# Kernel tuning notes

Hardware: AMD Instinct MI355X
Metric: run time of the kernel (lower is better)

## Reference

```python
import jax, jax.numpy as jnp
import numpy as np
import math

B, T, D, H, DM = 2, 2048, 1024, 16, 256
DK = D // H

def setup_inputs() -> dict:
    key = jax.random.key(0)
    ks = jax.random.split(key, 13)
    s = 0.02
    return {
        "Hx": jax.random.normal(ks[0], (B, D, T, 1), jnp.float32),
        "Hf": jax.random.normal(ks[1], (B, T, D), jnp.float32),
        "Gm": jax.random.normal(ks[2], (B, T, DM), jnp.float32),
        "Wg": jax.random.normal(ks[3], (T, DM), jnp.float32) * s,
        "bg": jax.random.normal(ks[4], (T,), jnp.float32) * s,
        "Wq": jax.random.normal(ks[5], (D, 2 * D), jnp.float32) * s,
        "bq": jax.random.normal(ks[6], (D,), jnp.float32) * s,
        "Wk": jax.random.normal(ks[7], (D, 2 * D), jnp.float32) * s,
        "bk": jax.random.normal(ks[8], (D,), jnp.float32) * s,
        "Wv": jax.random.normal(ks[9], (D, D), jnp.float32) * s,
        "bv": jax.random.normal(ks[10], (D,), jnp.float32) * s,
        "Wo": jax.random.normal(ks[11], (D, D), jnp.float32) * s,
        "bo": jax.random.normal(ks[12], (D,), jnp.float32) * s,
    }

def reference(Hx, Hf, Gm, Wg, bg, Wq, bq, Wk, bk, Wv, bv, Wo, bo):
    # Hx: (B, D, T, 1) -> (B, T, D)
    hx = jnp.transpose(Hx[..., 0], (0, 2, 1))
    h_cat = jnp.concatenate([hx, Hf], axis=-1)          # (B, T, 2D)
    Q = h_cat @ Wq.T + bq                               # (B, T, D)
    K = h_cat @ Wk.T + bk
    V = hx @ Wv.T + bv
    # split heads: (B, H, T, DK)
    Q = Q.reshape(B, T, H, DK).transpose(0, 2, 1, 3)
    K = K.reshape(B, T, H, DK).transpose(0, 2, 1, 3)
    V = V.reshape(B, T, H, DK).transpose(0, 2, 1, 3)
    scores = jnp.einsum('bhqd,bhkd->bhqk', Q, K) / math.sqrt(DK)
    bias = Gm @ Wg.T + bg                                # (B, T, T)
    scores = scores + bias[:, None, :, :]
    attn = jax.nn.softmax(scores, axis=-1)
    out = jnp.einsum('bhqk,bhkd->bhqd', attn, V)
    out = out.transpose(0, 2, 1, 3).reshape(B, T, D)
    return out @ Wo.T + bo
```

## Files before the change

### kernel.cpp

```cpp
#include <hip/hip_runtime.h>
#include <hip/hip_bf16.h>

using bf16 = __hip_bfloat16;
typedef __attribute__((ext_vector_type(8))) __bf16 bf16x8;
typedef __attribute__((ext_vector_type(4))) float f32x4;

#define GLB_AS(p) ((const __attribute__((address_space(1))) unsigned int*)(p))
#define LDS_AS(p) ((__attribute__((address_space(3))) unsigned int*)(p))

__device__ __forceinline__ void async_copy16(const void* g, void* l) {
  __builtin_amdgcn_global_load_lds(GLB_AS(g), LDS_AS(l), 16, 0, 0);
}

__device__ __forceinline__ f32x4 mfma16x16x32(bf16x8 a, bf16x8 b, f32x4 c) {
  return __builtin_amdgcn_mfma_f32_16x16x32_bf16(a, b, c, 0, 0, 0);
}

__device__ __forceinline__ float bfu2f(unsigned short u) {
  union { unsigned int i; float f; } x;
  x.i = (unsigned int)u << 16;
  return x.f;
}

#define LOG2E 1.44269504f

__global__ __launch_bounds__(256) void pack_hx(const float* __restrict__ Hx,
                                               bf16* __restrict__ hcat) {
  __shared__ float tile[64][65];
  const int t0 = blockIdx.x * 64, d0 = blockIdx.y * 64, b = blockIdx.z;
  const int c = threadIdx.x & 63, r0 = threadIdx.x >> 6;
#pragma unroll
  for (int i = 0; i < 16; ++i) {
    const int rd = r0 + i * 4;
    tile[rd][c] = Hx[((size_t)(b * 1024 + d0 + rd)) * 2048 + t0 + c];
  }
  __syncthreads();
#pragma unroll
  for (int i = 0; i < 16; ++i) {
    const int ct = r0 + i * 4;
    hcat[((size_t)(b * 2048 + t0 + ct)) * 2048 + d0 + c] =
        __float2bfloat16(tile[c][ct]);
  }
}

__global__ __launch_bounds__(256) void pack_all(
    const float* __restrict__ Hf, const float* __restrict__ Wq,
    const float* __restrict__ Wk, const float* __restrict__ Wv,
    const float* __restrict__ Wo, const float* __restrict__ Wg,
    const float* __restrict__ Gm, const float* __restrict__ bq,
    const float* __restrict__ bk, const float* __restrict__ bv,
    bf16* __restrict__ hcat, bf16* __restrict__ Wqkvb, bf16* __restrict__ Wob,
    bf16* __restrict__ Wgb, bf16* __restrict__ Gmb,
    float* __restrict__ qkvbias) {
  const int gid = blockIdx.x * 256 + threadIdx.x;
  const float* src = nullptr;
  bf16* dst = nullptr;
  int lg = 0, ldo = 0, off = 0, idx = 0;
  bool zero = false;
  if (gid < 1048576) { idx = gid; src = Hf; dst = hcat; lg = 8; ldo = 2048; off = 1024; }
  else if (gid < 1572864) { idx = gid - 1048576; src = Wq; dst = Wqkvb; lg = 9; ldo = 2048; }
  else if (gid < 2097152) { idx = gid - 1572864; src = Wk; dst = Wqkvb + (size_t)1024 * 2048; lg = 9; ldo = 2048; }
  else if (gid < 2359296) { idx = gid - 2097152; src = Wv; dst = Wqkvb + (size_t)2048 * 2048; lg = 8; ldo = 2048; }
  else if (gid < 2621440) { idx = gid - 2359296; zero = true; dst = Wqkvb + (size_t)2048 * 2048 + 1024; lg = 8; ldo = 2048; }
  else if (gid < 2883584) { idx = gid - 2621440; src = Wo; dst = Wob; lg = 8; ldo = 1024; }
  else if (gid < 3014656) { idx = gid - 2883584; src = Wg; dst = Wgb; lg = 6; ldo = 256; }
  else if (gid < 3276800) { idx = gid - 3014656; src = Gm; dst = Gmb; lg = 6; ldo = 256; }
  else if (gid < 3277056) { const int i = gid - 3276800; ((float4*)qkvbias)[i] = ((const float4*)bq)[i]; return; }
  else if (gid < 3277312) { const int i = gid - 3277056; ((float4*)(qkvbias + 1024))[i] = ((const float4*)bk)[i]; return; }
  else { const int i = gid - 3277312; ((float4*)(qkvbias + 2048))[i] = ((const float4*)bv)[i]; return; }
  const int row = idx >> lg, c = idx & ((1 << lg) - 1);
  bf16* o = dst + (size_t)row * ldo + off + c * 4;
  __align__(8) bf16 tmp[4];
  if (zero) {
    tmp[0] = tmp[1] = tmp[2] = tmp[3] = __float2bfloat16(0.f);
  } else {
    const float4 v = ((const float4*)src)[(size_t)idx];
    tmp[0] = __float2bfloat16(v.x); tmp[1] = __float2bfloat16(v.y);
    tmp[2] = __float2bfloat16(v.z); tmp[3] = __float2bfloat16(v.w);
  }
  *(ushort4*)o = *(const ushort4*)tmp;
}

__global__ __launch_bounds__(512, 2) void gemm_qkv_bias(
    const bf16* __restrict__ hcat, const bf16* __restrict__ Wqkv,
    const float* __restrict__ qkvbias, const bf16* __restrict__ Gmb,
    const bf16* __restrict__ Wgb, const float* __restrict__ bg,
    bf16* __restrict__ QKb, bf16* __restrict__ Vt, bf16* __restrict__ biasS) {
  __shared__ __align__(16) bf16 AS[2][256][64];
  __shared__ __align__(16) bf16 BS[2][256][64];
  const int lin = blockIdx.x;
  const bool isqkv = lin < 192;
  int m0, n0, Kd, KT, nit2;
  const bf16 *Ag, *Bg;
  const float* biasv;
  if (isqkv) {
    const int xcd = lin & 7, kk = lin >> 3;
    const int mloc = kk / 6, nloc = kk - mloc * 6;
    m0 = ((xcd >> 1) * 4 + mloc) * 256;
    n0 = ((xcd & 1) * 6 + nloc) * 256;
    Ag = hcat; Bg = Wqkv; biasv = qkvbias;
    Kd = 2048; KT = 32; nit2 = 16;
  } else {
    const int l2 = lin - 192;
    m0 = (l2 >> 3) * 256;
    n0 = (l2 & 7) * 256;
    Ag = Gmb; Bg = Wgb; biasv = bg;
    Kd = 256; KT = 4; nit2 = 2;
  }
  const int tid = threadIdx.x, lane = tid & 63, w = tid >> 6;
  const int w8 = w * 8, ln3 = lane >> 3, ch = lane & 7;
  const int fr = lane & 15, ck = lane >> 4;
  const int wm64 = (w >> 2) * 64;
  const int wn32 = (w & 3) * 32;

  f32x4 acc[8][4];
  const f32x4 fzero = {0.f, 0.f, 0.f, 0.f};
#pragma unroll
  for (int i = 0; i < 8; ++i)
#pragma unroll
    for (int j = 0; j < 4; ++j) acc[i][j] = fzero;

  auto stageA = [&](int buf, int mh, int kt) {
    const int k0 = kt * 64;
#pragma unroll
    for (int l = 0; l < 2; ++l) {
      const int rit = mh * 128 + l * 64 + w8 + ln3;
      async_copy16(Ag + (size_t)(m0 + rit) * Kd + k0 + ((ch ^ ln3) << 3),
                   (char*)&AS[buf][0][0] + ((mh * 128 + l * 64 + w8) << 7));
    }
  };
  auto stageB = [&](int buf, int nh, int kt) {
    const int k0 = kt * 64;
#pragma unroll
    for (int l = 0; l < 2; ++l) {
      const int rit = nh * 128 + l * 64 + w8 + ln3;
      async_copy16(Bg + (size_t)(n0 + rit) * Kd + k0 + ((ch ^ ln3) << 3),
                   (char*)&BS[buf][0][0] + ((nh * 128 + l * 64 + w8) << 7));
    }
  };

  bf16x8 af[4][2], bA[2][2], bB[2][2];
  auto ldA = [&](int buf, int mh) {
#pragma unroll
    for (int i = 0; i < 4; ++i)
#pragma unroll
      for (int ks = 0; ks < 2; ++ks)
        af[i][ks] = *(const bf16x8*)(
            &AS[buf][mh * 128 + wm64 + i * 16 + fr][0] +
            (((ks * 4 + ck) ^ (fr & 7)) << 3));
  };
  auto ldB = [&](bf16x8 (&dst)[2][2], int buf, int nh) {
#pragma unroll
    for (int j = 0; j < 2; ++j)
#pragma unroll
      for (int ks = 0; ks < 2; ++ks)
        dst[j][ks] = *(const bf16x8*)(
            &BS[buf][nh * 128 + wn32 + j * 16 + fr][0] +
            (((ks * 4 + ck) ^ (fr & 7)) << 3));
  };

#define BAR() __builtin_amdgcn_s_barrier()
#define LGKM0() asm volatile("s_waitcnt lgkmcnt(0)" ::: "memory")
#define MMAQ(MH, NH, BF)                                                      \
  __builtin_amdgcn_s_setprio(1);                                              \
  _Pragma("unroll") for (int i_ = 0; i_ < 4; ++i_) {                          \
    _Pragma("unroll") for (int j_ = 0; j_ < 2; ++j_) {                        \
      acc[(MH) * 4 + i_][(NH) * 2 + j_] = mfma16x16x32(                       \
          af[i_][0], BF[j_][0], acc[(MH) * 4 + i_][(NH) * 2 + j_]);           \
      acc[(MH) * 4 + i_][(NH) * 2 + j_] = mfma16x16x32(                       \
          af[i_][1], BF[j_][1], acc[(MH) * 4 + i_][(NH) * 2 + j_]);           \
    }                                                                         \
  }                                                                           \
  __builtin_amdgcn_s_setprio(0);

  stageA(0, 0, 0); stageB(0, 0, 0); stageB(0, 1, 0); stageA(0, 1, 0);
  stageA(1, 0, 1); stageB(1, 0, 1);
  asm volatile("s_waitcnt vmcnt(4)" ::: "memory");
  BAR();

  for (int it = 0; it < nit2; ++it) {
    const int kodd = 2 * it + 1;
    const int kn0 = (2 * it + 2 < KT) ? 2 * it + 2 : KT - 1;
    const int kn1 = (2 * it + 3 < KT) ? 2 * it + 3 : KT - 1;

    ldA(0, 0); ldB(bA, 0, 0);
    stageB(1, 1, kodd);
    asm volatile("s_waitcnt lgkmcnt(8)");
    BAR(); LGKM0();
    MMAQ(0, 0, bA);
    BAR();
    ldB(bB, 0, 1);
    stageA(1, 1, kodd);
    BAR(); LGKM0();
    MMAQ(0, 1, bB);
    BAR();
    ldA(0, 1);
    stageA(0, 0, kn0);
    BAR(); LGKM0();
    MMAQ(1, 0, bA);
    BAR();
    stageB(0, 0, kn0);
    asm volatile("s_waitcnt vmcnt(4)" ::: "memory");
    BAR();
    MMAQ(1, 1, bB);
    BAR();
    ldA(1, 0); ldB(bA, 1, 0);
    stageB(0, 1, kn0);
    asm volatile("s_waitcnt lgkmcnt(8)");
    BAR(); LGKM0();
    MMAQ(0, 0, bA);
    BAR();
    ldB(bB, 1, 1);
    stageA(0, 1, kn0);
    BAR(); LGKM0();
    MMAQ(0, 1, bB);
    BAR();
    ldA(1, 1);
    stageA(1, 0, kn1);
    BAR(); LGKM0();
    MMAQ(1, 0, bA);
    BAR();
    stageB(1, 0, kn1);
    asm volatile("s_waitcnt vmcnt(4)" ::: "memory");
    BAR();
    MMAQ(1, 1, bB);
    BAR();
  }
  asm volatile("s_waitcnt vmcnt(0)" ::: "memory");

  const int erow = (lane >> 4) * 4, ecol = lane & 15;
  if (!isqkv) {
#pragma unroll
    for (int ai = 0; ai < 8; ++ai) {
      const int gm0 = m0 + (ai >> 2) * 128 + wm64 + (ai & 3) * 16 + erow;
#pragma unroll
      for (int bj = 0; bj < 4; ++bj) {
        const int gn = n0 + (bj >> 1) * 128 + wn32 + (bj & 1) * 16 + ecol;
        const float bv = biasv[gn];
#pragma unroll
        for (int r = 0; r < 4; ++r)
          biasS[(size_t)(gm0 + r) * 2048 + gn] =
              __float2bfloat16((acc[ai][bj][r] + bv) * LOG2E);
      }
    }
  } else if (n0 < 2048) {
    const float sc = (n0 < 1024) ? 0.125f * LOG2E : 1.0f;
#pragma unroll
    for (int ai = 0; ai < 8; ++ai) {
      const int gm0 = m0 + (ai >> 2) * 128 + wm64 + (ai & 3) * 16 + erow;
#pragma unroll
      for (int bj = 0; bj < 4; ++bj) {
        const int gn = n0 + (bj >> 1) * 128 + wn32 + (bj & 1) * 16 + ecol;
        const float bv = biasv[gn];
#pragma unroll
        for (int r = 0; r < 4; ++r)
          QKb[(size_t)(gm0 + r) * 2048 + gn] =
              __float2bfloat16((acc[ai][bj][r] + bv) * sc);
      }
    }
  } else {
#pragma unroll
    for (int ai = 0; ai < 8; ++ai) {
      const int gm0 = m0 + (ai >> 2) * 128 + wm64 + (ai & 3) * 16 + erow;
      const int bb = gm0 >> 11;
      const int t = gm0 & 2047;
#pragma unroll
      for (int bj = 0; bj < 4; ++bj) {
        const int gn = n0 + (bj >> 1) * 128 + wn32 + (bj & 1) * 16 + ecol;
        const float bv = biasv[gn];
        const int d = gn - 2048;
        __align__(8) bf16 tmp[4];
#pragma unroll
        for (int r = 0; r < 4; ++r)
          tmp[r] = __float2bfloat16(acc[ai][bj][r] + bv);
        *(ushort4*)(Vt + ((size_t)(bb * 1024 + d)) * 2048 + t) =
            *(const ushort4*)tmp;
      }
    }
  }
#undef MMAQ
#undef LGKM0
#undef BAR
}

__global__ __launch_bounds__(256) void gemm_out(const bf16* __restrict__ A,
                                                const bf16* __restrict__ W,
                                                const float* __restrict__ biasv,
                                                float* __restrict__ C) {
  __shared__ __align__(16) bf16 As[2][128 * 64];
  __shared__ __align__(16) bf16 Bs[2][64 * 64];
  const int lin = blockIdx.x;
  const int xcd = lin & 7;
  const int kk = lin >> 3;
  const int m0 = (kk >> 1) * 128;
  const int n0 = (xcd * 2 + (kk & 1)) * 64;
  const int tid = threadIdx.x, lane = tid & 63, w = tid >> 6;
  const int wm = (w >> 1) * 64, wn = (w & 1) * 32;
  const int fr = lane & 15;
  const int ck = lane >> 4;

  f32x4 acc[4][2];
  const f32x4 fzero = {0.f, 0.f, 0.f, 0.f};
#pragma unroll
  for (int i = 0; i < 4; ++i)
#pragma unroll
    for (int j = 0; j < 2; ++j) acc[i][j] = fzero;

  auto stage = [&](int it, int buf) {
    const int k0 = it * 64;
#pragma unroll
    for (int is = 0; is < 4; ++is) {
      const int off = is * 4096 + w * 1024;
      const int row = (off >> 7) + (lane >> 3);
      const int sch = ((lane & 7) ^ (row & 7)) * 8;
      async_copy16(A + (size_t)(m0 + row) * 1024 + k0 + sch,
                   (char*)As[buf] + off);
      if (is < 2)
        async_copy16(W + (size_t)(n0 + row) * 1024 + k0 + sch,
                     (char*)Bs[buf] + off);
    }
  };

  stage(0, 0);
  __syncthreads();
  for (int it = 0; it < 16; ++it) {
    const int cur = it & 1;
    if (it + 1 < 16) stage(it + 1, cur ^ 1);
#pragma unroll
    for (int ks = 0; ks < 2; ++ks) {
      bf16x8 af[4], bfr[2];
      const int swk0 = (((ks * 4 + ck) ^ (fr & 7))) * 8;
#pragma unroll
      for (int i = 0; i < 4; ++i)
        af[i] = *(const bf16x8*)(As[cur] + (wm + i * 16 + fr) * 64 + swk0);
#pragma unroll
      for (int j = 0; j < 2; ++j)
        bfr[j] = *(const bf16x8*)(Bs[cur] + (wn + j * 16 + fr) * 64 + swk0);
#pragma unroll
      for (int i = 0; i < 4; ++i)
#pragma unroll
        for (int j = 0; j < 2; ++j)
          acc[i][j] = mfma16x16x32(af[i], bfr[j], acc[i][j]);
    }
    __syncthreads();
  }
  const int erow = (lane >> 4) * 4;
  const int ecol = lane & 15;
#pragma unroll
  for (int i = 0; i < 4; ++i) {
    const int gm0 = m0 + wm + i * 16 + erow;
#pragma unroll
    for (int j = 0; j < 2; ++j) {
      const int gn = n0 + wn + j * 16 + ecol;
      const float bv = biasv[gn];
#pragma unroll
      for (int r = 0; r < 4; ++r)
        C[(size_t)(gm0 + r) * 1024 + gn] = acc[i][j][r] + bv;
    }
  }
}

__global__ __launch_bounds__(256) void flash_attn(
    const bf16* __restrict__ Qm, const bf16* __restrict__ Km,
    const bf16* __restrict__ Vtm, const bf16* __restrict__ biasS,
    float* __restrict__ Op0, float* __restrict__ Op1,
    float* __restrict__ lpart) {
  __shared__ __align__(16) bf16 Ks[2][2][64 * 64];
  __shared__ __align__(16) bf16 Vs[2][64 * 64];
  __shared__ __align__(16) bf16 Ps[4 * 32 * 72];
  const int lin = blockIdx.x;
  const int xcd = lin & 7;
  const int kk = lin >> 3;
  const int cl = kk & 1;
  const int r2 = kk >> 1;
  const int half = r2 & 1;
  const int q0 = (r2 >> 1) * 128;
  const int combo = xcd * 2 + cl;
  const int hp = combo & 7;
  const int b = combo >> 3;
  const int tid = threadIdx.x, lane = tid & 63, w = tid >> 6;
  const int ql = lane & 15, qk = lane >> 4;
  const int T = 2048, D = 1024;
  const int sw0 = (qk ^ (ql & 7)) * 8;
  const int sw1 = ((qk + 4) ^ (ql & 7)) * 8;
  const int ln3 = lane >> 3;
  const int sch = ((lane & 7) ^ ln3) << 3;
  const int jb = half * 16;

  bf16x8 qf[2][2][2];
#pragma unroll
  for (int hh = 0; hh < 2; ++hh)
#pragma unroll
    for (int qt = 0; qt < 2; ++qt)
#pragma unroll
      for (int ks = 0; ks < 2; ++ks)
        qf[hh][qt][ks] = *(const bf16x8*)(
            Qm + (size_t)(b * T + q0 + w * 32 + qt * 16 + ql) * 2048 +
            (hp * 2 + hh) * 64 + ks * 32 + qk * 8);

  f32x4 acc[2][4][2];
  const f32x4 fzero = {0.f, 0.f, 0.f, 0.f};
#pragma unroll
  for (int hh = 0; hh < 2; ++hh)
#pragma unroll
    for (int dt = 0; dt < 4; ++dt)
#pragma unroll
      for (int qt = 0; qt < 2; ++qt) acc[hh][dt][qt] = fzero;
  float lp[2][2] = {{0.f, 0.f}, {0.f, 0.f}};

  const bf16* kbase0 = Km + (size_t)(b * T) * 2048 + (hp * 2) * 64;
  const bf16* vbase0 = Vtm + (size_t)(b * D + hp * 2 * 64) * 2048;
  const bf16* bb0 = biasS + (size_t)(b * T + q0 + w * 32 + ql) * 2048 + qk * 4;
  bf16* pb = Ps + w * 2304;

  ushort4 bqA[2][4], bqB[2][4];

#pragma unroll
  for (int hh = 0; hh < 2; ++hh)
#pragma unroll
    for (int is = 0; is < 2; ++is) {
      const int off = is * 4096 + w * 1024;
      const int row = is * 32 + w * 8 + ln3;
      async_copy16(kbase0 + (size_t)(jb * 64 + row) * 2048 + hh * 64 + sch,
                   (char*)Ks[0][hh] + off);
    }
#pragma unroll
  for (int qt = 0; qt < 2; ++qt)
#pragma unroll
    for (int jt = 0; jt < 4; ++jt)
      bqA[qt][jt] =
          *(const ushort4*)(bb0 + (size_t)qt * 16 * 2048 + jb * 64 + jt * 16);

#define QKHEAD(HH, CUR, BQC)                                                   \
  {                                                                            \
    const bf16* ksp_ = Ks[CUR][HH];                                            \
    _Pragma("unroll") for (int jt_ = 0; jt_ < 4; ++jt_) {                      \
      const bf16x8 kf0_ = *(const bf16x8*)(ksp_ + (jt_ * 16 + ql) * 64 + sw0); \
      const bf16x8 kf1_ = *(const bf16x8*)(ksp_ + (jt_ * 16 + ql) * 64 + sw1); \
      _Pragma("unroll") for (int qt_ = 0; qt_ < 2; ++qt_) {                    \
        f32x4 c_;                                                              \
        c_[0] = bfu2f(BQC[qt_][jt_].x); c_[1] = bfu2f(BQC[qt_][jt_].y);        \
        c_[2] = bfu2f(BQC[qt_][jt_].z); c_[3] = bfu2f(BQC[qt_][jt_].w);        \
        c_ = mfma16x16x32(kf0_, qf[HH][qt_][0], c_);                           \
        c_ = mfma16x16x32(kf1_, qf[HH][qt_][1], c_);                           \
        __align__(8) bf16 t4_[4];                                              \
        _Pragma("unroll") for (int r_ = 0; r_ < 4; ++r_) {                     \
          const float pv_ = __builtin_amdgcn_exp2f(c_[r_]);                    \
          lp[HH][qt_] += pv_;                                                  \
          t4_[r_] = __float2bfloat16(pv_);                                     \
        }                                                                      \
        *(ushort4*)(pb + (qt_ * 16 + ql) * 72 + jt_ * 16 + qk * 4) =           \
            *(const ushort4*)t4_;                                              \
      }                                                                        \
    }                                                                          \
  }

#define PVHEAD(HH)                                                             \
  {                                                                            \
    const bf16* vsp_ = Vs[HH];                                                 \
    __builtin_amdgcn_s_setprio(1);                                             \
    _Pragma("unroll") for (int ks_ = 0; ks_ < 2; ++ks_) {                      \
      const bf16x8 pf0_ = *(const bf16x8*)(pb + ql * 72 + ks_ * 32 + qk * 8);  \
      const bf16x8 pf1_ =                                                      \
          *(const bf16x8*)(pb + (16 + ql) * 72 + ks_ * 32 + qk * 8);           \
      const int sw_ = ks_ ? sw1 : sw0;                                         \
      _Pragma("unroll") for (int dt_ = 0; dt_ < 4; ++dt_) {                    \
        const bf16x8 vf_ =                                                     \
            *(const bf16x8*)(vsp_ + (dt_ * 16 + ql) * 64 + sw_);               \
        acc[HH][dt_][0] = mfma16x16x32(pf0_, vf_, acc[HH][dt_][0]);            \
        acc[HH][dt_][1] = mfma16x16x32(pf1_, vf_, acc[HH][dt_][1]);            \
      }                                                                        \
    }                                                                          \
    __builtin_amdgcn_s_setprio(0);                                             \
  }

#define AITER(JV, CUR, BQC, BQN)                                               \
  {                                                                            \
    const int j_ = (JV);                                                       \
    const int jn_ = j_ < 15 ? j_ + 1 : 15;  \
    const int jjc_ = jb + j_, jjn_ = jb + jn_;                                 \
    _Pragma("unroll") for (int hh_ = 0; hh_ < 2; ++hh_)                        \
        _Pragma("unroll") for (int is_ = 0; is_ < 2; ++is_) {                  \
      const int off_ = is_ * 4096 + w * 1024;                                  \
      const int row_ = is_ * 32 + w * 8 + ln3;                                 \
      async_copy16(                                                            \
          kbase0 + (size_t)(jjn_ * 64 + row_) * 2048 + hh_ * 64 + sch,         \
          (char*)Ks[(CUR) ^ 1][hh_] + off_);                                   \
    }                                                                          \
    _Pragma("unroll") for (int hh_ = 0; hh_ < 2; ++hh_)                        \
        _Pragma("unroll") for (int is_ = 0; is_ < 2; ++is_) {                  \
      const int off_ = is_ * 4096 + w * 1024;                                  \
      const int row_ = is_ * 32 + w * 8 + ln3;                                 \
      async_copy16(                                                            \
          vbase0 + (size_t)(hh_ * 64 + row_) * 2048 + jjc_ * 64 + sch,         \
          (char*)Vs[hh_] + off_);                                              \
    }                                                                          \
    _Pragma("unroll") for (int qt_ = 0; qt_ < 2; ++qt_)                        \
        _Pragma("unroll") for (int jt_ = 0; jt_ < 4; ++jt_)                    \
            BQN[qt_][jt_] = *(const ushort4*)(bb0 + (size_t)qt_ * 16 * 2048 +  \
                                              jjn_ * 64 + jt_ * 16);           \
    asm volatile("s_waitcnt vmcnt(16)" ::: "memory");                          \
    __builtin_amdgcn_s_barrier();                                              \
    QKHEAD(0, CUR, BQC)                                                        \
    asm volatile("s_waitcnt vmcnt(8)" ::: "memory");                           \
    __builtin_amdgcn_s_barrier();                                              \
    PVHEAD(0)                                                                  \
    QKHEAD(1, CUR, BQC)                                                        \
    PVHEAD(1)                                                                  \
    __builtin_amdgcn_s_barrier();                                              \
  }

  for (int jp = 0; jp < 8; ++jp) {
    AITER(jp * 2, 0, bqA, bqB)
    AITER(jp * 2 + 1, 1, bqB, bqA)
  }
#undef AITER
#undef QKHEAD
#undef PVHEAD
  asm volatile("s_waitcnt vmcnt(0)" ::: "memory");

#pragma unroll
  for (int hh = 0; hh < 2; ++hh)
#pragma unroll
    for (int qt = 0; qt < 2; ++qt) {
      lp[hh][qt] += __shfl_xor(lp[hh][qt], 16);
      lp[hh][qt] += __shfl_xor(lp[hh][qt], 32);
    }
  if (qk == 0) {
#pragma unroll
    for (int hh = 0; hh < 2; ++hh)
#pragma unroll
      for (int qt = 0; qt < 2; ++qt)
        lpart[half * 65536 + (b * 16 + hp * 2 + hh) * 2048 + q0 + w * 32 +
              qt * 16 + ql] = lp[hh][qt];
  }
  float* Op = half ? Op1 : Op0;
#pragma unroll
  for (int hh = 0; hh < 2; ++hh)
#pragma unroll
    for (int qt = 0; qt < 2; ++qt)
#pragma unroll
      for (int r = 0; r < 4; ++r) {
        const size_t orow =
            (size_t)(b * T + q0 + w * 32 + qt * 16 + qk * 4 + r);
#pragma unroll
        for (int dt = 0; dt < 4; ++dt)
          Op[orow * 1024 + (hp * 2 + hh) * 64 + dt * 16 + ql] =
              acc[hh][dt][qt][r];
      }
}

__global__ __launch_bounds__(256) void combine(const float* __restrict__ O0,
                                               const float* __restrict__ O1,
                                               const float* __restrict__ lpart,
                                               bf16* __restrict__ AOut) {
  const int idx = blockIdx.x * 256 + threadIdx.x;
  const int row = idx >> 8;
  const int col = (idx & 255) * 4;
  const int b = row >> 11, q = row & 2047, h = col >> 6;
  const int li = (b * 16 + h) * 2048 + q;
  const float inv = __builtin_amdgcn_rcpf(lpart[li] + lpart[65536 + li]);
  const float4 a = *(const float4*)(O0 + (size_t)row * 1024 + col);
  const float4 c = *(const float4*)(O1 + (size_t)row * 1024 + col);
  __align__(8) bf16 t[4] = {
      __float2bfloat16((a.x + c.x) * inv), __float2bfloat16((a.y + c.y) * inv),
      __float2bfloat16((a.z + c.z) * inv), __float2bfloat16((a.w + c.w) * inv)};
  *(ushort4*)(AOut + (size_t)row * 1024 + col) = *(const ushort4*)t;
}

extern "C" void kernel_launch(void* const* d_in, const int* in_sizes, int n_in,
                              void* d_out, int out_size, void* d_ws,
                              size_t ws_size, hipStream_t stream) {
  (void)in_sizes; (void)n_in; (void)out_size; (void)ws_size;
  const float* Hx = (const float*)d_in[0];
  const float* Hf = (const float*)d_in[1];
  const float* Gm = (const float*)d_in[2];
  const float* Wg = (const float*)d_in[3];
  const float* bg = (const float*)d_in[4];
  const float* Wq = (const float*)d_in[5];
  const float* bq = (const float*)d_in[6];
  const float* Wk = (const float*)d_in[7];
  const float* bk = (const float*)d_in[8];
  const float* Wv = (const float*)d_in[9];
  const float* bv = (const float*)d_in[10];
  const float* Wo = (const float*)d_in[11];
  const float* bo = (const float*)d_in[12];
  float* out = (float*)d_out;

  char* p = (char*)d_ws;
  bf16* hcat = (bf16*)p;   p += (size_t)4096 * 2048 * 2;
  bf16* QKb = (bf16*)p;    p += (size_t)4096 * 2048 * 2;
  bf16* Vtb = (bf16*)p;    p += (size_t)4096 * 1024 * 2;
  bf16* biasS = (bf16*)p;  p += (size_t)4096 * 2048 * 2;
  bf16* AOut = (bf16*)p;   p += (size_t)4096 * 1024 * 2;
  bf16* Wqkvb = (bf16*)p;  p += (size_t)3072 * 2048 * 2;
  bf16* Wob = (bf16*)p;    p += (size_t)1024 * 1024 * 2;
  bf16* Wgb = (bf16*)p;    p += (size_t)2048 * 256 * 2;
  bf16* Gmb = (bf16*)p;    p += (size_t)4096 * 256 * 2;
  float* qkvbias = (float*)p; p += (size_t)3072 * 4;
  float* Op1 = (float*)p;  p += (size_t)4096 * 1024 * 4;
  float* lpart = (float*)p; p += (size_t)2 * 65536 * 4;
  float* Op0 = (float*)hcat;

  pack_hx<<<dim3(32, 16, 2), 256, 0, stream>>>(Hx, hcat);
  pack_all<<<dim3(12803), 256, 0, stream>>>(Hf, Wq, Wk, Wv, Wo, Wg, Gm, bq, bk,
                                            bv, hcat, Wqkvb, Wob, Wgb, Gmb,
                                            qkvbias);
  gemm_qkv_bias<<<dim3(320), 512, 0, stream>>>(hcat, Wqkvb, qkvbias, Gmb,
                                               Wgb, bg, QKb, Vtb, biasS);
  flash_attn<<<dim3(512), 256, 0, stream>>>(QKb, QKb + 1024, Vtb, biasS,
                                            Op0, Op1, lpart);
  combine<<<dim3(4096), 256, 0, stream>>>(Op0, Op1, lpart, AOut);
  gemm_out<<<dim3(512), 256, 0, stream>>>(AOut, Wob, bo, out);
}
```

Baseline: 311.6 us.

## Use 512-thread flash-attention blocks with double-buffered K and V tiles

The flash attention kernel now runs 8 waves per block covering 256 query rows instead of 4 waves covering 128, and the grid is halved. Each K/V tile loaded into LDS is therefore shared by twice as many query rows. V now gets its own double buffer and is prefetched together with the next K tile, which removes the mid-iteration wait and barrier between the QK and PV phases. The block index mapping changes from an XCD-aware layout to a plain head-major one. The cost is more LDS per block and fewer blocks to spread across CUs, and the loss of the XCD-aware mapping may hurt cache locality.

```diff
diff --git a/kernel.cpp b/kernel.cpp
--- a/kernel.cpp
+++ b/kernel.cpp
@@ -360,24 +360,20 @@
   }
 }
 
-__global__ __launch_bounds__(256) void flash_attn(
+__global__ __launch_bounds__(512, 2) void flash_attn(
     const bf16* __restrict__ Qm, const bf16* __restrict__ Km,
     const bf16* __restrict__ Vtm, const bf16* __restrict__ biasS,
     float* __restrict__ Op0, float* __restrict__ Op1,
     float* __restrict__ lpart) {
   __shared__ __align__(16) bf16 Ks[2][2][64 * 64];
-  __shared__ __align__(16) bf16 Vs[2][64 * 64];
-  __shared__ __align__(16) bf16 Ps[4 * 32 * 72];
+  __shared__ __align__(16) bf16 Vs[2][2][64 * 64];
+  __shared__ __align__(16) bf16 Ps[8 * 32 * 72];
   const int lin = blockIdx.x;
-  const int xcd = lin & 7;
-  const int kk = lin >> 3;
-  const int cl = kk & 1;
-  const int r2 = kk >> 1;
-  const int half = r2 & 1;
-  const int q0 = (r2 >> 1) * 128;
-  const int combo = xcd * 2 + cl;
-  const int hp = combo & 7;
-  const int b = combo >> 3;
+  const int hp = lin >> 5;
+  const int g = lin & 31;
+  const int half = g & 1;
+  const int b = (g >> 1) & 1;
+  const int q0 = (g >> 2) * 256;
   const int tid = threadIdx.x, lane = tid & 63, w = tid >> 6;
   const int ql = lane & 15, qk = lane >> 4;
   const int T = 2048, D = 1024;
@@ -412,18 +408,19 @@
   const bf16* vbase0 = Vtm + (size_t)(b * D + hp * 2 * 64) * 2048;
   const bf16* bb0 = biasS + (size_t)(b * T + q0 + w * 32 + ql) * 2048 + qk * 4;
   bf16* pb = Ps + w * 2304;
+  const int srow = w * 8 + ln3;
 
   ushort4 bqA[2][4], bqB[2][4];
 
-#pragma unroll
-  for (int hh = 0; hh < 2; ++hh)
-#pragma unroll
-    for (int is = 0; is < 2; ++is) {
-      const int off = is * 4096 + w * 1024;
-      const int row = is * 32 + w * 8 + ln3;
-      async_copy16(kbase0 + (size_t)(jb * 64 + row) * 2048 + hh * 64 + sch,
-                   (char*)Ks[0][hh] + off);
-    }
+#define STAGEKV(BUF, JJ)                                                       \
+  _Pragma("unroll") for (int hh_ = 0; hh_ < 2; ++hh_) {                        \
+    async_copy16(kbase0 + (size_t)((JJ) * 64 + srow) * 2048 + hh_ * 64 + sch,  \
+                 (char*)Ks[BUF][hh_] + w * 1024);                              \
+    async_copy16(vbase0 + (size_t)(hh_ * 64 + srow) * 2048 + (JJ) * 64 + sch,  \
+                 (char*)Vs[BUF][hh_] + w * 1024);                              \
+  }
+
+  STAGEKV(0, jb)
 #pragma unroll
   for (int qt = 0; qt < 2; ++qt)
 #pragma unroll
@@ -455,9 +452,9 @@
     }                                                                          \
   }
 
-#define PVHEAD(HH)                                                             \
+#define PVHEAD(HH, CUR)                                                        \
   {                                                                            \
-    const bf16* vsp_ = Vs[HH];                                                 \
+    const bf16* vsp_ = Vs[CUR][HH];                                            \
     __builtin_amdgcn_s_setprio(1);                                             \
     _Pragma("unroll") for (int ks_ = 0; ks_ < 2; ++ks_) {                      \
       const bf16x8 pf0_ = *(const bf16x8*)(pb + ql * 72 + ks_ * 32 + qk * 8);  \
@@ -476,37 +473,19 @@
 
 #define AITER(JV, CUR, BQC, BQN)                                               \
   {                                                                            \
-    const int j_ = (JV);                                                       \
-    const int jn_ = j_ < 15 ? j_ + 1 : 15;  \
-    const int jjc_ = jb + j_, jjn_ = jb + jn_;                                 \
-    _Pragma("unroll") for (int hh_ = 0; hh_ < 2; ++hh_)                        \
-        _Pragma("unroll") for (int is_ = 0; is_ < 2; ++is_) {                  \
-      const int off_ = is_ * 4096 + w * 1024;                                  \
-      const int row_ = is_ * 32 + w * 8 + ln3;                                 \
-      async_copy16(                                                            \
-          kbase0 + (size_t)(jjn_ * 64 + row_) * 2048 + hh_ * 64 + sch,         \
-          (char*)Ks[(CUR) ^ 1][hh_] + off_);                                   \
-    }                                                                          \
-    _Pragma("unroll") for (int hh_ = 0; hh_ < 2; ++hh_)                        \
-        _Pragma("unroll") for (int is_ = 0; is_ < 2; ++is_) {                  \
-      const int off_ = is_ * 4096 + w * 1024;                                  \
-      const int row_ = is_ * 32 + w * 8 + ln3;                                 \
-      async_copy16(                                                            \
-          vbase0 + (size_t)(hh_ * 64 + row_) * 2048 + jjc_ * 64 + sch,         \
-          (char*)Vs[hh_] + off_);                                              \
-    }                                                                          \
+    const int jn_ = (JV) < 15 ? (JV) + 1 : 15;                                 \
+    const int jjn_ = jb + jn_;                                                 \
+    STAGEKV((CUR) ^ 1, jjn_)                                                   \
     _Pragma("unroll") for (int qt_ = 0; qt_ < 2; ++qt_)                        \
         _Pragma("unroll") for (int jt_ = 0; jt_ < 4; ++jt_)                    \
             BQN[qt_][jt_] = *(const ushort4*)(bb0 + (size_t)qt_ * 16 * 2048 +  \
                                               jjn_ * 64 + jt_ * 16);           \
-    asm volatile("s_waitcnt vmcnt(16)" ::: "memory");                          \
+    asm volatile("s_waitcnt vmcnt(12)" ::: "memory");                          \
     __builtin_amdgcn_s_barrier();                                              \
     QKHEAD(0, CUR, BQC)                                                        \
-    asm volatile("s_waitcnt vmcnt(8)" ::: "memory");                           \
-    __builtin_amdgcn_s_barrier();                                              \
-    PVHEAD(0)                                                                  \
+    PVHEAD(0, CUR)                                                             \
     QKHEAD(1, CUR, BQC)                                                        \
-    PVHEAD(1)                                                                  \
+    PVHEAD(1, CUR)                                                             \
     __builtin_amdgcn_s_barrier();                                              \
   }
 
@@ -517,6 +496,7 @@
 #undef AITER
 #undef QKHEAD
 #undef PVHEAD
+#undef STAGEKV
   asm volatile("s_waitcnt vmcnt(0)" ::: "memory");
 
 #pragma unroll
@@ -608,7 +588,7 @@
                                             qkvbias);
   gemm_qkv_bias<<<dim3(320), 512, 0, stream>>>(hcat, Wqkvb, qkvbias, Gmb,
                                                Wgb, bg, QKb, Vtb, biasS);
-  flash_attn<<<dim3(512), 256, 0, stream>>>(QKb, QKb + 1024, Vtb, biasS,
+  flash_attn<<<dim3(256), 512, 0, stream>>>(QKb, QKb + 1024, Vtb, biasS,
                                             Op0, Op1, lpart);
   combine<<<dim3(4096), 256, 0, stream>>>(Op0, Op1, lpart, AOut);
   gemm_out<<<dim3(512), 256, 0, stream>>>(AOut, Wob, bo, out);
```

New measurement: 280.3 us. -10.1%, faster.
